# Performance work log

Measured on AMD Instinct MI355X. Metric: run time of the kernel, lower is better.

## Reference

```python
import jax, jax.numpy as jnp
import numpy as np

B, N_PROP = 2, 512
C_FEAT, FH, FW = 256, 200, 200
NUM_CLASSES, NUM_STAGES = 81, 3
POOL, SR, SCALE = 7, 2, 0.25
IMG_H, IMG_W = 800.0, 800.0
FC_DIM = 1024
IN_DIM = C_FEAT * POOL * POOL
STDS = ((0.1, 0.1, 0.2, 0.2), (0.05, 0.05, 0.1, 0.1), (0.033, 0.033, 0.067, 0.067))
CLIP_VAL = float(np.log(1000.0 / 16))
SCORE_T, NMS_T, DETS, PRE_NMS = 0.05, 0.5, 100, 2048


def bilinear(f, y, x):
    # f: [C,H,W]; y,x: [M] sample coords (torchvision roi_align bilinear rules)
    H, W = f.shape[1], f.shape[2]
    valid = (y > -1.0) & (y < H) & (x > -1.0) & (x < W)
    y = jnp.clip(y, 0.0, H - 1.0)
    x = jnp.clip(x, 0.0, W - 1.0)
    y0 = jnp.floor(y).astype(jnp.int32)
    x0 = jnp.floor(x).astype(jnp.int32)
    y1 = jnp.minimum(y0 + 1, H - 1)
    x1 = jnp.minimum(x0 + 1, W - 1)
    ly, lx = y - y0, x - x0
    hy, hx = 1.0 - ly, 1.0 - lx
    v = (hy * hx) * f[:, y0, x0] + (hy * lx) * f[:, y0, x1] \
      + (ly * hx) * f[:, y1, x0] + (ly * lx) * f[:, y1, x1]
    return v * valid  # [C,M]


def roi_align(f, rois):
    # f: [C,H,W], rois: [N,4] image coords -> [N,C,POOL,POOL]
    b = rois * SCALE
    x1, y1, x2, y2 = b[:, 0], b[:, 1], b[:, 2], b[:, 3]
    rw = jnp.maximum(x2 - x1, 1.0)
    rh = jnp.maximum(y2 - y1, 1.0)
    bw, bh = rw / POOL, rh / POOL
    p = jnp.arange(POOL, dtype=f.dtype)
    s = (jnp.arange(SR, dtype=f.dtype) + 0.5) / SR
    gy = y1[:, None, None] + (p[None, :, None] + s[None, None, :]) * bh[:, None, None]  # [N,P,SR]
    gx = x1[:, None, None] + (p[None, :, None] + s[None, None, :]) * bw[:, None, None]
    n = rois.shape[0]
    yy = jnp.broadcast_to(gy[:, :, :, None, None], (n, POOL, SR, POOL, SR))
    xx = jnp.broadcast_to(gx[:, None, None, :, :], (n, POOL, SR, POOL, SR))
    vals = bilinear(f, yy.reshape(-1), xx.reshape(-1))  # [C, N*P*SR*P*SR]
    vals = vals.reshape(f.shape[0], n, POOL, SR, POOL, SR).mean(axis=(3, 5))
    return vals.transpose(1, 0, 2, 3)


def decode_clip(props, deltas, stds):
    px1, py1, px2, py2 = props[:, 0], props[:, 1], props[:, 2], props[:, 3]
    pw = jnp.maximum(px2 - px1, 1e-6)
    ph = jnp.maximum(py2 - py1, 1e-6)
    px = px1 + 0.5 * pw
    py = py1 + 0.5 * ph
    wx, wy, ww, wh = stds
    dx = deltas[:, 0] * wx
    dy = deltas[:, 1] * wy
    dw = jnp.minimum(deltas[:, 2] * ww, CLIP_VAL)
    dh = jnp.minimum(deltas[:, 3] * wh, CLIP_VAL)
    gx = dx * pw + px
    gy = dy * ph + py
    gw = jnp.exp(dw) * pw
    gh = jnp.exp(dh) * ph
    return jnp.stack([jnp.clip(gx - 0.5 * gw, 0.0, IMG_W),
                      jnp.clip(gy - 0.5 * gh, 0.0, IMG_H),
                      jnp.clip(gx + 0.5 * gw, 0.0, IMG_W),
                      jnp.clip(gy + 0.5 * gh, 0.0, IMG_H)], axis=1)


def box_iou(a, b):
    area_a = (a[:, 2] - a[:, 0]) * (a[:, 3] - a[:, 1])
    area_b = (b[:, 2] - b[:, 0]) * (b[:, 3] - b[:, 1])
    lt = jnp.maximum(a[:, None, :2], b[None, :, :2])
    rb = jnp.minimum(a[:, None, 2:], b[None, :, 2:])
    wh = jnp.maximum(rb - lt, 0.0)
    inter = wh[..., 0] * wh[..., 1]
    return inter / (area_a[:, None] + area_b[None, :] - inter + 1e-12)


def postprocess(boxes, probs):
    # boxes [N,4], probs [N,NUM_CLASSES] -> fixed-size padded detections
    n = boxes.shape[0]
    ws = boxes[:, 2] - boxes[:, 0]
    hs = boxes[:, 3] - boxes[:, 1]
    ok = (ws >= 1.0) & (hs >= 1.0)  # remove_small_boxes(min_size=1.0)
    fg = probs[:, 1:]               # drop background (class 0)
    sc = jnp.where((fg > SCORE_T) & ok[:, None], fg, -1.0).reshape(-1)  # [N*(C-1)]
    labels = jnp.broadcast_to(jnp.arange(1, NUM_CLASSES, dtype=jnp.int32)[None, :],
                              (n, NUM_CLASSES - 1)).reshape(-1)
    bflat = jnp.broadcast_to(boxes[:, None, :], (n, NUM_CLASSES - 1, 4)).reshape(-1, 4)
    vals, idx = jax.lax.top_k(sc, PRE_NMS)  # fixed-size candidate cap, sorted desc
    bsel = bflat[idx]
    lsel = labels[idx]
    # batched_nms trick: offset boxes per label so classes never overlap
    off = bsel + (lsel.astype(bsel.dtype) * (jnp.max(bsel) + 1.0))[:, None]
    iou = box_iou(off, off)
    valid = vals > 0.0
    ar = jnp.arange(PRE_NMS)
    def body(i, keep):
        sup = (iou[i] > NMS_T) & keep[i]
        return keep & ~(sup & (ar > i))
    keep = jax.lax.fori_loop(0, PRE_NMS, body, valid)
    order = jnp.argsort(jnp.where(keep, ar, PRE_NMS + ar))[:DETS]  # kept first, score order
    kv = keep[order]
    out_boxes = jnp.where(kv[:, None], bsel[order], 0.0)
    out_scores = jnp.where(kv, vals[order], 0.0)
    out_labels = jnp.where(kv, lsel[order], 0)
    return out_boxes, out_scores, out_labels


def cascade_forward(features, proposals, W1, b1, W2, b2, Wc, bc, Wr, br):
    cur = proposals  # [B,N,4]
    logits = None
    for s in range(NUM_STAGES):
        pooled = jax.vmap(roi_align)(features, cur)  # [B,N,C,P,P]
        x = pooled.reshape(B * N_PROP, IN_DIM)
        h = jax.nn.relu(x @ W1[s] + b1[s])
        h = jax.nn.relu(h @ W2[s] + b2[s])
        logits = h @ Wc[s] + bc[s]
        deltas = (h @ Wr[s] + br[s]).reshape(B, N_PROP, 4)
        stds = STDS[s]
        cur = jax.vmap(lambda p, d: decode_clip(p, d, stds))(cur, deltas)
    probs = jax.nn.softmax(logits, axis=-1).reshape(B, N_PROP, NUM_CLASSES)
    return jax.vmap(postprocess)(cur, probs)


def setup_inputs() -> dict:
    key = jax.random.key(0)
    ks = jax.random.split(key, 12)
    features = jax.random.normal(ks[0], (B, C_FEAT, FH, FW), jnp.float32)
    cx = jax.random.uniform(ks[1], (B, N_PROP), minval=0.0, maxval=IMG_W)
    cy = jax.random.uniform(ks[2], (B, N_PROP), minval=0.0, maxval=IMG_H)
    w = jax.random.uniform(ks[3], (B, N_PROP), minval=16.0, maxval=256.0)
    h = jax.random.uniform(ks[4], (B, N_PROP), minval=16.0, maxval=256.0)
    proposals = jnp.stack([jnp.clip(cx - w / 2, 0.0, IMG_W), jnp.clip(cy - h / 2, 0.0, IMG_H),
                           jnp.clip(cx + w / 2, 0.0, IMG_W), jnp.clip(cy + h / 2, 0.0, IMG_H)],
                          axis=-1)
    def lin(k, fan_in, shape):
        return jax.random.normal(k, shape, jnp.float32) / np.sqrt(fan_in).astype(np.float32)
    W1 = lin(ks[5], IN_DIM, (NUM_STAGES, IN_DIM, FC_DIM))
    W2 = lin(ks[6], FC_DIM, (NUM_STAGES, FC_DIM, FC_DIM))
    Wc = lin(ks[7], FC_DIM, (NUM_STAGES, FC_DIM, NUM_CLASSES))
    Wr = lin(ks[8], FC_DIM, (NUM_STAGES, FC_DIM, 4)) * 0.5
    b1 = jnp.zeros((NUM_STAGES, FC_DIM), jnp.float32)
    b2 = jnp.zeros((NUM_STAGES, FC_DIM), jnp.float32)
    bc = jnp.zeros((NUM_STAGES, NUM_CLASSES), jnp.float32)
    br = jnp.zeros((NUM_STAGES, 4), jnp.float32)
    return {"features": features, "proposals": proposals, "W1": W1, "b1": b1,
            "W2": W2, "b2": b2, "Wc": Wc, "bc": bc, "Wr": Wr, "br": br}


def reference(features, proposals, W1, b1, W2, b2, Wc, bc, Wr, br):
    return cascade_forward(features, proposals, W1, b1, W2, b2, Wc, bc, Wr, br)
```

## Files before the change

kernel.cpp:

```cpp
#include <hip/hip_runtime.h>
#include <float.h>
#include <math.h>

#define NB 2
#define NPROP 512
#define NROI 1024
#define CFEAT 256
#define FH 200
#define FW 200
#define HWSZ 40000
#define INDIM 12544
#define FCD 1024
#define NCLS 81
#define NCAND 40960
#define CAP 4096
#define NSEL 2048
#define DETS 100
#define CLIPV 4.135166556742356f

#define KKT1 392
#define KKT2 32

typedef __attribute__((ext_vector_type(8))) short short8v;
typedef __attribute__((ext_vector_type(8))) unsigned short ushort8v;
typedef __attribute__((ext_vector_type(4))) float float4v;

__device__ __forceinline__ unsigned short f2bf(float x) {
    unsigned u = __float_as_uint(x);
    unsigned r = (u + 0x7fffu + ((u >> 16) & 1u)) >> 16;
    return (unsigned short)r;
}
__device__ __forceinline__ float bf2f(unsigned short b) {
    return __uint_as_float(((unsigned)b) << 16);
}
__device__ __forceinline__ void split3(float x, unsigned short& h, unsigned short& m, unsigned short& l) {
    h = f2bf(x);
    float r1 = x - bf2f(h);
    m = f2bf(r1);
    float r2 = r1 - bf2f(m);
    l = f2bf(r2);
}

__device__ __forceinline__ void gload_lds16(const void* g, void* l) {
    __builtin_amdgcn_global_load_lds((const __attribute__((address_space(1))) unsigned int*)g,
                                     (__attribute__((address_space(3))) unsigned int*)l, 16, 0, 0);
}

__device__ __forceinline__ int swz8k(int o) {
    return o ^ ((((o >> 6) ^ (o >> 8)) & 3) << 4);
}

__global__ void zero_ints_k(int* p, int n) {
    int i = blockIdx.x * blockDim.x + threadIdx.x;
    if (i < n) p[i] = 0;
}

__global__ __launch_bounds__(256) void transpose_k(const float* __restrict__ in, float* __restrict__ out) {
    __shared__ float tile[32][33];
    int b = blockIdx.z;
    int hw0 = blockIdx.x * 32;
    int c0 = blockIdx.y * 32;
    int tx = threadIdx.x;
    int ty = threadIdx.y;
#pragma unroll
    for (int i = 0; i < 32; i += 8)
        tile[ty + i][tx] = in[((size_t)(b * CFEAT + c0 + ty + i)) * HWSZ + hw0 + tx];
    __syncthreads();
#pragma unroll
    for (int i = 0; i < 32; i += 8)
        out[((size_t)b * HWSZ + hw0 + ty + i) * CFEAT + c0 + tx] = tile[tx][ty + i];
}

template<bool TRANS>
__device__ __forceinline__ float bil_sample(const float* __restrict__ feat, int b, int c,
                                            float yy, float xx) {
    bool valid = (yy > -1.f) && (yy < (float)FH) && (xx > -1.f) && (xx < (float)FW);
    float yc = fminf(fmaxf(yy, 0.f), (float)(FH - 1));
    float xc = fminf(fmaxf(xx, 0.f), (float)(FW - 1));
    int y0 = (int)floorf(yc), x0 = (int)floorf(xc);
    int y1i = min(y0 + 1, FH - 1), x1i = min(x0 + 1, FW - 1);
    float ly = yc - (float)y0, lx = xc - (float)x0;
    float hy = 1.f - ly, hx = 1.f - lx;
    float v00, v01, v10, v11;
    if (TRANS) {
        const float* base = feat + (size_t)b * HWSZ * CFEAT;
        v00 = base[((size_t)(y0 * FW + x0)) * CFEAT + c];
        v01 = base[((size_t)(y0 * FW + x1i)) * CFEAT + c];
        v10 = base[((size_t)(y1i * FW + x0)) * CFEAT + c];
        v11 = base[((size_t)(y1i * FW + x1i)) * CFEAT + c];
    } else {
        const float* base = feat + ((size_t)(b * CFEAT + c)) * HWSZ;
        v00 = base[y0 * FW + x0];
        v01 = base[y0 * FW + x1i];
        v10 = base[y1i * FW + x0];
        v11 = base[y1i * FW + x1i];
    }
    float v = hy * hx * v00 + hy * lx * v01 + ly * hx * v10 + ly * lx * v11;
    return valid ? v : 0.f;
}

template<bool TRANS>
__global__ __launch_bounds__(256) void roi_k(const float* __restrict__ feat,
                                             const float* __restrict__ boxes,
                                             float* __restrict__ xout) {
    int pp = blockIdx.x, r = blockIdx.y, c = threadIdx.x;
    int b = r >> 9;
    const float* bx = boxes + (size_t)r * 4;
    float x1 = bx[0] * 0.25f, y1 = bx[1] * 0.25f, x2 = bx[2] * 0.25f, y2 = bx[3] * 0.25f;
    float rw = fmaxf(x2 - x1, 1.0f), rh = fmaxf(y2 - y1, 1.0f);
    float bw = rw / 7.0f, bh = rh / 7.0f;
    int py = pp / 7, px = pp % 7;
    float acc = 0.f;
#pragma unroll
    for (int sy = 0; sy < 2; ++sy)
#pragma unroll
        for (int sx = 0; sx < 2; ++sx)
            acc += bil_sample<TRANS>(feat, b, c,
                                     y1 + ((float)py + 0.25f + 0.5f * (float)sy) * bh,
                                     x1 + ((float)px + 0.25f + 0.5f * (float)sx) * bw);
    xout[(size_t)r * INDIM + pp * 256 + c] = acc * 0.25f;
}

__global__ __launch_bounds__(256) void roi_split4_k(const float* __restrict__ feat,
                                                    const float* __restrict__ boxes,
                                                    unsigned short* __restrict__ Ap) {
    int tid = threadIdx.x;
    int g = tid >> 7;
    int binhalf = (tid >> 6) & 1;
    int cl = tid & 63;
    int r = blockIdx.x * 2 + g;
    int b = r >> 9;
    const float* bx = boxes + (size_t)r * 4;
    float x1 = bx[0] * 0.25f, y1 = bx[1] * 0.25f, x2 = bx[2] * 0.25f, y2 = bx[3] * 0.25f;
    float rw = fmaxf(x2 - x1, 1.0f), rh = fmaxf(y2 - y1, 1.0f);
    float bw = rw / 7.0f, bh = rh / 7.0f;
    int mt = r >> 7, rr = r & 127;
    size_t pstr = (size_t)8 * KKT1 * 4096;
    const float* base = feat + (size_t)b * HWSZ * CFEAT;
    for (int pp = binhalf; pp < 49; pp += 2) {
        int py = pp / 7, px = pp % 7;
        float ax = 0.f, ay = 0.f, az = 0.f, aw = 0.f;
#pragma unroll
        for (int sy = 0; sy < 2; ++sy) {
#pragma unroll
            for (int sx = 0; sx < 2; ++sx) {
                float yy = y1 + ((float)py + 0.25f + 0.5f * (float)sy) * bh;
                float xx = x1 + ((float)px + 0.25f + 0.5f * (float)sx) * bw;
                bool valid = (yy > -1.f) && (yy < (float)FH) && (xx > -1.f) && (xx < (float)FW);
                float yc = fminf(fmaxf(yy, 0.f), (float)(FH - 1));
                float xc = fminf(fmaxf(xx, 0.f), (float)(FW - 1));
                int y0 = (int)floorf(yc), x0 = (int)floorf(xc);
                int y1i = min(y0 + 1, FH - 1), x1i = min(x0 + 1, FW - 1);
                float ly = yc - (float)y0, lx = xc - (float)x0;
                float hy = 1.f - ly, hx = 1.f - lx;
                float w00 = hy * hx, w01 = hy * lx, w10 = ly * hx, w11 = ly * lx;
                if (!valid) { w00 = w01 = w10 = w11 = 0.f; }
                float4 v00 = ((const float4*)(base + (size_t)(y0 * FW + x0) * CFEAT))[cl];
                float4 v01 = ((const float4*)(base + (size_t)(y0 * FW + x1i) * CFEAT))[cl];
                float4 v10 = ((const float4*)(base + (size_t)(y1i * FW + x0) * CFEAT))[cl];
                float4 v11 = ((const float4*)(base + (size_t)(y1i * FW + x1i) * CFEAT))[cl];
                ax += w00 * v00.x + w01 * v01.x + w10 * v10.x + w11 * v11.x;
                ay += w00 * v00.y + w01 * v01.y + w10 * v10.y + w11 * v11.y;
                az += w00 * v00.z + w01 * v01.z + w10 * v10.z + w11 * v11.z;
                aw += w00 * v00.w + w01 * v01.w + w10 * v10.w + w11 * v11.w;
            }
        }
        ax *= 0.25f; ay *= 0.25f; az *= 0.25f; aw *= 0.25f;
        ushort4 h4, m4, l4;
        split3(ax, h4.x, m4.x, l4.x);
        split3(ay, h4.y, m4.y, l4.y);
        split3(az, h4.z, m4.z, l4.z);
        split3(aw, h4.w, m4.w, l4.w);
        int k0 = pp * 256 + cl * 4;
        int kk = k0 >> 5;
        size_t tile = ((size_t)mt * KKT1 + kk) * 4096 + rr * 32 + (k0 & 31);
        *(ushort4*)&Ap[tile] = h4;
        *(ushort4*)&Ap[tile + pstr] = m4;
        *(ushort4*)&Ap[tile + 2 * pstr] = l4;
    }
}

template<bool PERM>
__global__ __launch_bounds__(256) void wsplit_k(const float* __restrict__ W,
                                                unsigned short* __restrict__ out, int kkT) {
    __shared__ float tf[32][132];
    int nt = blockIdx.x, kk = blockIdx.y;
    int t = threadIdx.x;
    int kloc = t >> 3;
    int f4 = t & 7;
    int krow;
    if (PERM) krow = ((kk & 7) * 32 + kloc) * 49 + (kk >> 3);
    else krow = kk * 32 + kloc;
    const float* src = W + (size_t)krow * 1024 + nt * 128;
#pragma unroll
    for (int q = 0; q < 4; ++q) {
        float4 v = *(const float4*)(src + (f4 + q * 8) * 4);
        *(float4*)&tf[kloc][(f4 + q * 8) * 4] = v;
    }
    __syncthreads();
    int r = t >> 1;
    size_t tileBase = ((size_t)nt * kkT + kk) * 4096;
    size_t pstr = (size_t)8 * kkT * 4096;
#pragma unroll
    for (int cc = 0; cc < 2; ++cc) {
        int c = (t & 1) * 2 + cc;
        ushort8v hv, mv, lv;
#pragma unroll
        for (int e = 0; e < 8; ++e) {
            unsigned short h, m, l;
            split3(tf[c * 8 + e][r], h, m, l);
            hv[e] = h; mv[e] = m; lv[e] = l;
        }
        size_t o = tileBase + r * 32 + c * 8;
        *(ushort8v*)&out[o] = hv;
        *(ushort8v*)&out[o + pstr] = mv;
        *(ushort8v*)&out[o + 2 * pstr] = lv;
    }
}

__global__ __launch_bounds__(256) void wsplit_head_k(const float* __restrict__ Wc,
                                                     const float* __restrict__ Wr,
                                                     unsigned short* __restrict__ out) {
    int kk = blockIdx.x, t = threadIdx.x;
    int r = t >> 1;
    int k0 = (t & 1) * 16;
    size_t pstr = (size_t)KKT2 * 4096;
    for (int e = 0; e < 16; ++e) {
        int k = k0 + e;
        int krow = kk * 32 + k;
        float v = 0.f;
        if (r < 81) v = Wc[(size_t)krow * 81 + r];
        else if (r < 85) v = Wr[(size_t)krow * 4 + (r - 81)];
        unsigned short h, m, l;
        split3(v, h, m, l);
        size_t o = (size_t)kk * 4096 + r * 32 + k;
        out[o] = h;
        out[o + pstr] = m;
        out[o + 2 * pstr] = l;
    }
}

#define TERM16(AF) { _Pragma("unroll") for (int i = 0; i < 4; ++i) _Pragma("unroll") \
    for (int j = 0; j < 4; ++j) acc[i][j] = __builtin_amdgcn_mfma_f32_16x16x32_bf16(AF[i], bf[j], acc[i][j], 0, 0, 0); }

__global__ __launch_bounds__(256) void gemm_mfma_k(const unsigned short* __restrict__ Ap,
                                                   const unsigned short* __restrict__ Bp,
                                                   float* __restrict__ partial,
                                                   int kkT, int kkPer, int NT, int N) {
    __shared__ unsigned short sA[3][4096];
    __shared__ unsigned short sB[3][4096];
    int tid = threadIdx.x;
    int phys = blockIdx.x;
    int logical = (phys & 7) * (gridDim.x >> 3) + (phys >> 3);
    int tpc = 8 * NT;
    int xy = logical % tpc;
    int ck = logical / tpc;
    int mt = xy & 7, nt = xy >> 3;
    int kk0 = ck * kkPer;
    size_t pstrA = (size_t)8 * kkT * 4096 * 2;
    size_t pstrB = (size_t)NT * kkT * 4096 * 2;
    const char* aBase = (const char*)(Ap + (size_t)mt * kkT * 4096);
    const char* bBase = (const char*)(Bp + (size_t)nt * kkT * 4096);

    float4v acc[4][4];
#pragma unroll
    for (int i = 0; i < 4; ++i)
#pragma unroll
        for (int j = 0; j < 4; ++j) acc[i][j] = (float4v){0.f, 0.f, 0.f, 0.f};

    int lane = tid & 63, wv = tid >> 6;
    int wr = wv >> 1, wc = wv & 1;
    int ln = lane & 15;
    int q = lane >> 4;
    int qs = (q ^ (ln ^ (ln >> 2))) & 3;
    int aoffE = (wr * 64 + ln) * 32 + qs * 8;
    int boffE = (wc * 64 + ln) * 32 + qs * 8;

    int o0 = tid * 16;
    int o1 = o0 + 4096;
    int s0 = swz8k(o0);
    int s1 = swz8k(o1);

    for (int kk = kk0; kk < kk0 + kkPer; ++kk) {
        const char* at = aBase + (size_t)kk * 8192;
        const char* bt = bBase + (size_t)kk * 8192;
#pragma unroll
        for (int p = 0; p < 3; ++p) {
            gload_lds16(at + (size_t)p * pstrA + s0, (char*)sA[p] + o0);
            gload_lds16(at + (size_t)p * pstrA + s1, (char*)sA[p] + o1);
            gload_lds16(bt + (size_t)p * pstrB + s0, (char*)sB[p] + o0);
            gload_lds16(bt + (size_t)p * pstrB + s1, (char*)sB[p] + o1);
        }
        __syncthreads();
        short8v af[3][4];
#pragma unroll
        for (int p = 0; p < 3; ++p)
#pragma unroll
            for (int f = 0; f < 4; ++f)
                af[p][f] = *(const short8v*)&sA[p][aoffE + f * 512];
        short8v bf[4];
#pragma unroll
        for (int f = 0; f < 4; ++f) bf[f] = *(const short8v*)&sB[0][boffE + f * 512];
        TERM16(af[0]); TERM16(af[1]); TERM16(af[2]);
#pragma unroll
        for (int f = 0; f < 4; ++f) bf[f] = *(const short8v*)&sB[1][boffE + f * 512];
        TERM16(af[0]); TERM16(af[1]);
#pragma unroll
        for (int f = 0; f < 4; ++f) bf[f] = *(const short8v*)&sB[2][boffE + f * 512];
        TERM16(af[0]);
        __syncthreads();
    }
    float* outp = partial + (size_t)ck * 1024 * N;
    int row0 = mt * 128 + wr * 64 + (lane >> 4) * 4;
    int col = nt * 128 + wc * 64 + ln;
#pragma unroll
    for (int i = 0; i < 4; ++i)
#pragma unroll
        for (int j = 0; j < 4; ++j)
#pragma unroll
            for (int qq = 0; qq < 4; ++qq)
                outp[(size_t)(row0 + i * 16 + qq) * N + col + j * 16] = acc[i][j][qq];
}

template<int NS>
__global__ void reduce8_k(const float* __restrict__ partial, const float* __restrict__ bias,
                          unsigned short* __restrict__ planes) {
    int i = blockIdx.x * 256 + threadIdx.x;
    float s = 0.f;
#pragma unroll
    for (int c = 0; c < NS; ++c) s += partial[((size_t)c << 20) + i];
    s += bias[i & 1023];
    s = fmaxf(s, 0.f);
    int m = i >> 10, n = i & 1023;
    int mt = m >> 7, rr = m & 127, kk = n >> 5;
    unsigned short h, mm_, l;
    split3(s, h, mm_, l);
    size_t tile = ((size_t)mt * KKT2 + kk) * 4096 + rr * 32 + (n & 31);
    size_t pstr = (size_t)8 * KKT2 * 4096;
    planes[tile] = h;
    planes[tile + pstr] = mm_;
    planes[tile + 2 * pstr] = l;
}

__global__ void head_fin_k(const float* __restrict__ partial, const float* __restrict__ bc,
                           const float* __restrict__ br, float* __restrict__ logits,
                           float* __restrict__ deltas, int write_logits) {
    int idx = blockIdx.x * 256 + threadIdx.x;
    if (idx >= 1024 * 85) return;
    int m = idx / 85, col = idx - m * 85;
    float s = 0.f;
#pragma unroll
    for (int c = 0; c < 8; ++c) s += partial[(size_t)c * 131072 + m * 128 + col];
    if (col < 81) {
        if (write_logits) logits[(size_t)m * NCLS + col] = s + bc[col];
    } else {
        deltas[(size_t)m * 4 + (col - 81)] = s + br[col - 81];
    }
}

template<bool PERM>
__global__ __launch_bounds__(256) void gemm_k(const float* __restrict__ A,
                                              const float* __restrict__ Bm,
                                              float* __restrict__ partial,
                                              int K_total, int Kchunk) {
    const int M = 1024, N = 1024;
    __shared__ float As[2][16][128];
    __shared__ float Bs[2][16][64];
    int tid = threadIdx.x;
    int mb = blockIdx.x & 7;
    int nb = blockIdx.x >> 3;
    int ck = blockIdx.y;
    int k0 = ck * Kchunk;
    int am = tid >> 1;
    int ak = (tid & 1) * 8;
    int bk = tid >> 4;
    int bn = (tid & 15) * 4;
    int ty = tid >> 4, tx = tid & 15;
    const float* Aptr = A + (size_t)(mb * 128 + am) * K_total + k0 + ak;

    float acc[8][4];
#pragma unroll
    for (int i = 0; i < 8; ++i)
#pragma unroll
        for (int j = 0; j < 4; ++j) acc[i][j] = 0.f;

    auto bRowPtr = [&](int kk) -> const float* {
        int row = PERM ? ((kk & 255) * 49 + (kk >> 8)) : kk;
        return Bm + (size_t)row * N + nb * 64 + bn;
    };

    int T = Kchunk / 16;
    float4 a0 = *(const float4*)(Aptr);
    float4 a1 = *(const float4*)(Aptr + 4);
    float4 b0 = *(const float4*)bRowPtr(k0 + bk);
    As[0][ak + 0][am] = a0.x; As[0][ak + 1][am] = a0.y; As[0][ak + 2][am] = a0.z; As[0][ak + 3][am] = a0.w;
    As[0][ak + 4][am] = a1.x; As[0][ak + 5][am] = a1.y; As[0][ak + 6][am] = a1.z; As[0][ak + 7][am] = a1.w;
    *(float4*)&Bs[0][bk][bn] = b0;
    __syncthreads();

    int p = 0;
    for (int t = 0; t < T; ++t) {
        if (t + 1 < T) {
            a0 = *(const float4*)(Aptr + (t + 1) * 16);
            a1 = *(const float4*)(Aptr + (t + 1) * 16 + 4);
            b0 = *(const float4*)bRowPtr(k0 + (t + 1) * 16 + bk);
        }
#pragma unroll
        for (int k = 0; k < 16; ++k) {
            float4 av0 = *(const float4*)&As[p][k][ty * 8];
            float4 av1 = *(const float4*)&As[p][k][ty * 8 + 4];
            float4 bv = *(const float4*)&Bs[p][k][tx * 4];
            float ar[8] = {av0.x, av0.y, av0.z, av0.w, av1.x, av1.y, av1.z, av1.w};
            float br_[4] = {bv.x, bv.y, bv.z, bv.w};
#pragma unroll
            for (int i = 0; i < 8; ++i)
#pragma unroll
                for (int j = 0; j < 4; ++j) acc[i][j] = fmaf(ar[i], br_[j], acc[i][j]);
        }
        if (t + 1 < T) {
            __syncthreads();
            int qb = 1 - p;
            As[qb][ak + 0][am] = a0.x; As[qb][ak + 1][am] = a0.y; As[qb][ak + 2][am] = a0.z; As[qb][ak + 3][am] = a0.w;
            As[qb][ak + 4][am] = a1.x; As[qb][ak + 5][am] = a1.y; As[qb][ak + 6][am] = a1.z; As[qb][ak + 7][am] = a1.w;
            *(float4*)&Bs[qb][bk][bn] = b0;
            __syncthreads();
            p = qb;
        }
    }
    float* out = partial + ((size_t)ck * M + mb * 128 + ty * 8) * N + nb * 64 + tx * 4;
#pragma unroll
    for (int i = 0; i < 8; ++i) {
        float4 v = make_float4(acc[i][0], acc[i][1], acc[i][2], acc[i][3]);
        *(float4*)(out + (size_t)i * N) = v;
    }
}

__global__ void reduce4_k(const float* __restrict__ partial, const float* __restrict__ bias,
                          float* __restrict__ out) {
    const int MN = 1024 * 1024;
    int i = blockIdx.x * 256 + threadIdx.x;
    if (i >= MN) return;
    float s = partial[i] + partial[(size_t)MN + i] + partial[(size_t)2 * MN + i] + partial[(size_t)3 * MN + i];
    s += bias[i & 1023];
    out[i] = fmaxf(s, 0.f);
}

__global__ __launch_bounds__(128) void head_k(const float* __restrict__ h,
                                              const float* __restrict__ Wc, const float* __restrict__ bc,
                                              const float* __restrict__ Wr, const float* __restrict__ br,
                                              float* __restrict__ logits, float* __restrict__ deltas,
                                              int write_logits) {
    __shared__ float hs[1024];
    int m = blockIdx.x;
    int tid = threadIdx.x;
    const float4* hp = (const float4*)(h + (size_t)m * 1024);
    ((float4*)hs)[tid] = hp[tid];
    ((float4*)hs)[tid + 128] = hp[tid + 128];
    __syncthreads();
    int j = tid;
    if (j < 85) {
        bool is_cls = j < 81;
        const float* Wp = is_cls ? Wc : Wr;
        int stride = is_cls ? 81 : 4;
        int col = is_cls ? j : j - 81;
        float s0 = 0.f, s1 = 0.f, s2 = 0.f, s3 = 0.f;
        for (int k = 0; k < 1024; k += 4) {
            s0 = fmaf(hs[k + 0], Wp[(k + 0) * stride + col], s0);
            s1 = fmaf(hs[k + 1], Wp[(k + 1) * stride + col], s1);
            s2 = fmaf(hs[k + 2], Wp[(k + 2) * stride + col], s2);
            s3 = fmaf(hs[k + 3], Wp[(k + 3) * stride + col], s3);
        }
        float s = (s0 + s1) + (s2 + s3);
        if (is_cls) {
            if (write_logits) logits[(size_t)m * NCLS + col] = s + bc[col];
        } else {
            deltas[(size_t)m * 4 + col] = s + br[col];
        }
    }
}

__global__ void decode_k(const float* __restrict__ prev, const float* __restrict__ deltas,
                         float* __restrict__ nxt, float wx, float wy, float ww, float wh) {
    int r = blockIdx.x * 256 + threadIdx.x;
    if (r >= NROI) return;
    const float* p = prev + (size_t)r * 4;
    const float* d = deltas + (size_t)r * 4;
    float px1 = p[0], py1 = p[1], px2 = p[2], py2 = p[3];
    float pw = fmaxf(px2 - px1, 1e-6f), ph = fmaxf(py2 - py1, 1e-6f);
    float pcx = px1 + 0.5f * pw, pcy = py1 + 0.5f * ph;
    float dx = d[0] * wx, dy = d[1] * wy;
    float dw = fminf(d[2] * ww, CLIPV);
    float dh = fminf(d[3] * wh, CLIPV);
    float gx = dx * pw + pcx, gy = dy * ph + pcy;
    float gw = expf(dw) * pw, gh = expf(dh) * ph;
    nxt[(size_t)r * 4 + 0] = fminf(fmaxf(gx - 0.5f * gw, 0.f), 800.f);
    nxt[(size_t)r * 4 + 1] = fminf(fmaxf(gy - 0.5f * gh, 0.f), 800.f);
    nxt[(size_t)r * 4 + 2] = fminf(fmaxf(gx + 0.5f * gw, 0.f), 800.f);
    nxt[(size_t)r * 4 + 3] = fminf(fmaxf(gy + 0.5f * gh, 0.f), 800.f);
}

__global__ __launch_bounds__(128) void softmax_k(const float* __restrict__ logits, float* __restrict__ probs) {
    __shared__ float red[128];
    int m = blockIdx.x;
    int tid = threadIdx.x;
    float v = (tid < NCLS) ? logits[(size_t)m * NCLS + tid] : -FLT_MAX;
    red[tid] = v;
    __syncthreads();
    for (int o = 64; o; o >>= 1) {
        if (tid < o) red[tid] = fmaxf(red[tid], red[tid + o]);
        __syncthreads();
    }
    float mx = red[0];
    __syncthreads();
    float e = (tid < NCLS) ? expf(v - mx) : 0.f;
    red[tid] = e;
    __syncthreads();
    for (int o = 64; o; o >>= 1) {
        if (tid < o) red[tid] += red[tid + o];
        __syncthreads();
    }
    float s = red[0];
    if (tid < NCLS) probs[(size_t)m * NCLS + tid] = e / s;
}

__global__ void build_scores_k(const float* __restrict__ probs, const float* __restrict__ boxes,
                               float* __restrict__ sc, int* __restrict__ vcount) {
    int f = blockIdx.x * 256 + threadIdx.x;
    if (f >= NB * NCAND) return;
    int b = f / NCAND, ff = f % NCAND;
    int rr = ff / 80, cls = ff % 80 + 1;
    int row = b * NPROP + rr;
    const float* bx = boxes + (size_t)row * 4;
    bool ok = (bx[2] - bx[0] >= 1.f) && (bx[3] - bx[1] >= 1.f);
    float p = probs[(size_t)row * NCLS + cls];
    float s = (p > 0.05f && ok) ? p : -1.0f;
    sc[f] = s;
    if (s > 0.f) atomicAdd(&vcount[b], 1);
}

__global__ __launch_bounds__(1024) void find_pivot_k(const float* __restrict__ sc,
                                                     const int* __restrict__ vcount,
                                                     float* __restrict__ pivot) {
    int b = blockIdx.x;
    const float* s = sc + (size_t)b * NCAND;
    __shared__ int tot;
    int V = vcount[b];
    if (V <= CAP) {
        if (threadIdx.x == 0) pivot[b] = 0.f;
        return;
    }
    unsigned u = 0;
    for (int bit = 30; bit >= 0; --bit) {
        unsigned cand = u | (1u << bit);
        float cf = __uint_as_float(cand);
        if (threadIdx.x == 0) tot = 0;
        __syncthreads();
        int cnt = 0;
        for (int i = threadIdx.x; i < NCAND; i += 1024) cnt += (s[i] >= cf) ? 1 : 0;
        for (int o = 32; o; o >>= 1) cnt += __shfl_down(cnt, o);
        if ((threadIdx.x & 63) == 0) atomicAdd(&tot, cnt);
        __syncthreads();
        if (tot >= NSEL) u = cand;
        __syncthreads();
    }
    if (threadIdx.x == 0) pivot[b] = __uint_as_float(u);
}

__global__ void compact_k(const float* __restrict__ sc, const float* __restrict__ pivot,
                          float* __restrict__ ckey, int* __restrict__ cidx, int* __restrict__ ccount) {
    int f = blockIdx.x * 256 + threadIdx.x;
    if (f >= NB * NCAND) return;
    int b = f / NCAND, ff = f % NCAND;
    float s = sc[f];
    float pv = pivot[b];
    if (s > 0.f && s >= pv) {
        int slot = atomicAdd(&ccount[b], 1);
        if (slot < CAP) {
            ckey[(size_t)b * CAP + slot] = s;
            cidx[(size_t)b * CAP + slot] = ff;
        }
    }
}

__global__ __launch_bounds__(1024) void sort_select_k(const float* __restrict__ ckey,
                                                      const int* __restrict__ cidx,
                                                      const int* __restrict__ ccount,
                                                      const float* __restrict__ boxes,
                                                      float* __restrict__ selb, float* __restrict__ seloff,
                                                      float* __restrict__ selsc, int* __restrict__ sellab,
                                                      unsigned long long* __restrict__ vmask) {
    int b = blockIdx.x;
    __shared__ float ks[CAP];
    __shared__ int is[CAP];
    __shared__ float rmax[1024];
    int cnt = min(ccount[b], CAP);
    for (int i = threadIdx.x; i < CAP; i += 1024) {
        if (i < cnt) {
            ks[i] = ckey[(size_t)b * CAP + i];
            is[i] = cidx[(size_t)b * CAP + i];
        } else {
            ks[i] = -FLT_MAX;
            is[i] = 0x7FFFFFFF;
        }
    }
    __syncthreads();
    for (int k = 2; k <= CAP; k <<= 1) {
        for (int j = k >> 1; j > 0; j >>= 1) {
            for (int t = threadIdx.x; t < CAP; t += 1024) {
                int l = t ^ j;
                if (l > t) {
                    bool up = ((t & k) == 0);
                    float a = ks[t], bb = ks[l];
                    int ia = is[t], ib = is[l];
                    bool a_first = (a > bb) || (a == bb && ia < ib);
                    bool doswap = up ? !a_first : a_first;
                    if (doswap) {
                        ks[t] = bb; ks[l] = a;
                        is[t] = ib; is[l] = ia;
                    }
                }
            }
            __syncthreads();
        }
    }
    float lm = -FLT_MAX;
    for (int i = threadIdx.x; i < NSEL; i += 1024) {
        if (ks[i] > 0.f) {
            const float* bb = boxes + (size_t)(b * NPROP + is[i] / 80) * 4;
            lm = fmaxf(lm, fmaxf(fmaxf(bb[0], bb[1]), fmaxf(bb[2], bb[3])));
        }
    }
    rmax[threadIdx.x] = lm;
    __syncthreads();
    for (int o = 512; o; o >>= 1) {
        if (threadIdx.x < o) rmax[threadIdx.x] = fmaxf(rmax[threadIdx.x], rmax[threadIdx.x + o]);
        __syncthreads();
    }
    float maxb = (rmax[0] > -FLT_MAX) ? rmax[0] : 0.f;
    __syncthreads();
    for (int pass = 0; pass < 2; ++pass) {
        int i = pass * 1024 + threadIdx.x;
        bool v = ks[i] > 0.f;
        int idx = is[i];
        int rr = idx / 80;
        int cls = idx % 80 + 1;
        float b0 = 0.f, b1 = 0.f, b2 = 0.f, b3 = 0.f, offv = 0.f;
        if (v) {
            const float* bb = boxes + (size_t)(b * NPROP + rr) * 4;
            b0 = bb[0]; b1 = bb[1]; b2 = bb[2]; b3 = bb[3];
            offv = (maxb + 1.f) * (float)cls;
        }
        float* sb = selb + ((size_t)b * NSEL + i) * 4;
        sb[0] = b0; sb[1] = b1; sb[2] = b2; sb[3] = b3;
        float* so = seloff + ((size_t)b * NSEL + i) * 4;
        so[0] = b0 + offv; so[1] = b1 + offv; so[2] = b2 + offv; so[3] = b3 + offv;
        selsc[(size_t)b * NSEL + i] = v ? ks[i] : 0.f;
        sellab[(size_t)b * NSEL + i] = cls;
        unsigned long long m = __ballot(v);
        if ((threadIdx.x & 63) == 0) vmask[b * 32 + pass * 16 + (threadIdx.x >> 6)] = m;
    }
}

__global__ __launch_bounds__(256) void sup_k(const float* __restrict__ seloff,
                                             const float* __restrict__ selsc,
                                             unsigned long long* __restrict__ sup) {
    int b = blockIdx.y;
    int wave = threadIdx.x >> 6;
    int lane = threadIdx.x & 63;
    int pair = blockIdx.x * 4 + wave;
    int i = pair >> 5;
    int w = pair & 31;
    int j = w * 64 + lane;
    unsigned long long m = 0;
    if (selsc[(size_t)b * NSEL + i] > 0.f) {
        const float* oi = seloff + ((size_t)b * NSEL + i) * 4;
        const float* oj = seloff + ((size_t)b * NSEL + j) * 4;
        float ax1 = oi[0], ay1 = oi[1], ax2 = oi[2], ay2 = oi[3];
        float bx1 = oj[0], by1 = oj[1], bx2 = oj[2], by2 = oj[3];
        float areaA = (ax2 - ax1) * (ay2 - ay1);
        float areaB = (bx2 - bx1) * (by2 - by1);
        float ltx = fmaxf(ax1, bx1), lty = fmaxf(ay1, by1);
        float rbx = fminf(ax2, bx2), rby = fminf(ay2, by2);
        float iw = fmaxf(rbx - ltx, 0.f), ih = fmaxf(rby - lty, 0.f);
        float inter = iw * ih;
        float iou = inter / (areaA + areaB - inter + 1e-12f);
        m = __ballot(iou > 0.5f);
    }
    if (lane == 0) sup[((size_t)b * NSEL + i) * 32 + w] = m;
}

__global__ __launch_bounds__(256) void nms_scan_k(const unsigned long long* __restrict__ vmask,
                                                  const unsigned long long* __restrict__ sup,
                                                  const float* __restrict__ selb,
                                                  const float* __restrict__ selsc,
                                                  const int* __restrict__ sellab,
                                                  float* __restrict__ out) {
    int b = blockIdx.x;
    __shared__ unsigned long long keepw[32];
    __shared__ int pref[33];
    int tid = threadIdx.x;
    if (tid < 64) {
        int lane = tid;
        unsigned long long kw = (lane < 32) ? vmask[b * 32 + lane] : 0ull;
        for (int i = 0; i < NSEL; ++i) {
            int wi = i >> 6;
            unsigned long long wv = __shfl(kw, wi);
            if ((wv >> (i & 63)) & 1ull) {
                if (lane < 32) {
                    unsigned long long row = sup[((size_t)b * NSEL + i) * 32 + lane];
                    unsigned long long mask;
                    if (lane > wi) mask = ~0ull;
                    else if (lane == wi) mask = ((i & 63) == 63) ? 0ull : (~0ull << ((i & 63) + 1));
                    else mask = 0ull;
                    kw &= ~(row & mask);
                }
            }
        }
        if (lane < 32) keepw[lane] = kw;
    }
    __syncthreads();
    if (tid == 0) {
        int s = 0;
        for (int w = 0; w < 32; ++w) { pref[w] = s; s += __popcll(keepw[w]); }
        pref[32] = s;
    }
    __syncthreads();
    for (int i = tid; i < 600; i += 256) {
        if (i < 400) out[b * 400 + i] = 0.f;
        else if (i < 500) out[800 + b * 100 + (i - 400)] = 0.f;
        else out[1000 + b * 100 + (i - 500)] = 0.f;
    }
    __syncthreads();
    for (int e = tid; e < NSEL; e += 256) {
        int w = e >> 6;
        unsigned long long kw = keepw[w];
        if ((kw >> (e & 63)) & 1ull) {
            int rank = pref[w] + __popcll(kw & ((1ull << (e & 63)) - 1ull));
            if (rank < DETS) {
                const float* sb = selb + ((size_t)b * NSEL + e) * 4;
                out[b * 400 + rank * 4 + 0] = sb[0];
                out[b * 400 + rank * 4 + 1] = sb[1];
                out[b * 400 + rank * 4 + 2] = sb[2];
                out[b * 400 + rank * 4 + 3] = sb[3];
                out[800 + b * 100 + rank] = selsc[(size_t)b * NSEL + e];
                out[1000 + b * 100 + rank] = (float)sellab[(size_t)b * NSEL + e];
            }
        }
    }
}

extern "C" void kernel_launch(void* const* d_in, const int* in_sizes, int n_in,
                              void* d_out, int out_size, void* d_ws, size_t ws_size,
                              hipStream_t stream) {
    const float* features = (const float*)d_in[0];
    const float* proposals = (const float*)d_in[1];
    const float* W1 = (const float*)d_in[2];
    const float* b1 = (const float*)d_in[3];
    const float* W2 = (const float*)d_in[4];
    const float* b2 = (const float*)d_in[5];
    const float* Wc = (const float*)d_in[6];
    const float* bc = (const float*)d_in[7];
    const float* Wr = (const float*)d_in[8];
    const float* br = (const float*)d_in[9];

    char* ws = (char*)d_ws;
    size_t off = 0;
    auto alloc = [&](size_t bytes) -> void* {
        void* p = ws + off;
        off += (bytes + 255) & ~(size_t)255;
        return p;
    };

    float* logits = (float*)alloc((size_t)NROI * NCLS * 4);
    float* probs = (float*)alloc((size_t)NROI * NCLS * 4);
    float* deltas = (float*)alloc((size_t)NROI * 4 * 4);
    float* cur1 = (float*)alloc((size_t)NROI * 4 * 4);
    float* cur2 = (float*)alloc((size_t)NROI * 4 * 4);
    float* cur3 = (float*)alloc((size_t)NROI * 4 * 4);
    float* sc = (float*)alloc((size_t)NB * NCAND * 4);
    float* ckey = (float*)alloc((size_t)NB * CAP * 4);
    int* cidx = (int*)alloc((size_t)NB * CAP * 4);
    int* counters = (int*)alloc(256);
    float* pivot = (float*)(counters + 4);
    float* selb = (float*)alloc((size_t)NB * NSEL * 4 * 4);
    float* seloff = (float*)alloc((size_t)NB * NSEL * 4 * 4);
    float* selsc = (float*)alloc((size_t)NB * NSEL * 4);
    int* sellab = (int*)alloc((size_t)NB * NSEL * 4);
    unsigned long long* vmask = (unsigned long long*)alloc((size_t)NB * 32 * 8);
    unsigned long long* sup = (unsigned long long*)alloc((size_t)NB * NSEL * 32 * 8);

    const float stds[3][4] = {{0.1f, 0.1f, 0.2f, 0.2f},
                              {0.05f, 0.05f, 0.1f, 0.1f},
                              {0.033f, 0.033f, 0.067f, 0.067f}};
    float* curbufs[3] = {cur1, cur2, cur3};
    const float* curp = proposals;

    size_t planes1 = (size_t)3 * 8 * KKT1 * 4096 * 2;
    size_t planes2 = (size_t)3 * 8 * KKT2 * 4096 * 2;
    size_t planesH = (size_t)3 * 1 * KKT2 * 4096 * 2;
    auto mfma_need = [&](int sk) {
        return planes1 * 2 + planes2 * 3 + planesH +
               (size_t)sk * (1 << 20) * 4 +
               (size_t)NB * HWSZ * CFEAT * 4 + 65536;
    };
    int SK1 = 0;
    if (off + mfma_need(14) <= ws_size) SK1 = 14;
    else if (off + mfma_need(8) <= ws_size) SK1 = 8;

    zero_ints_k<<<1, 64, 0, stream>>>(counters, 4);

    if (SK1 > 0) {
        unsigned short* Ap1 = (unsigned short*)alloc(planes1);
        unsigned short* Bp1 = (unsigned short*)alloc(planes1);
        unsigned short* h1p = (unsigned short*)alloc(planes2);
        unsigned short* W2Tp = (unsigned short*)alloc(planes2);
        unsigned short* h2p = (unsigned short*)alloc(planes2);
        unsigned short* Whp = (unsigned short*)alloc(planesH);
        float* partial = (float*)alloc((size_t)SK1 * (1 << 20) * 4);
        float* featT = (float*)alloc((size_t)NB * HWSZ * CFEAT * 4);

        transpose_k<<<dim3(1250, 8, 2), dim3(32, 8), 0, stream>>>(features, featT);

        for (int s = 0; s < 3; ++s) {
            roi_split4_k<<<dim3(NROI / 2), 256, 0, stream>>>(featT, curp, Ap1);
            wsplit_k<true><<<dim3(8, KKT1), 256, 0, stream>>>(W1 + (size_t)s * INDIM * FCD, Bp1, KKT1);
            gemm_mfma_k<<<dim3(64 * SK1), 256, 0, stream>>>(Ap1, Bp1, partial, KKT1, KKT1 / SK1, 8, 1024);
            if (SK1 == 14)
                reduce8_k<14><<<4096, 256, 0, stream>>>(partial, b1 + s * FCD, h1p);
            else
                reduce8_k<8><<<4096, 256, 0, stream>>>(partial, b1 + s * FCD, h1p);
            wsplit_k<false><<<dim3(8, KKT2), 256, 0, stream>>>(W2 + (size_t)s * FCD * FCD, W2Tp, KKT2);
            gemm_mfma_k<<<dim3(512), 256, 0, stream>>>(h1p, W2Tp, partial, KKT2, 4, 8, 1024);
            reduce8_k<8><<<4096, 256, 0, stream>>>(partial, b2 + s * FCD, h2p);
            wsplit_head_k<<<dim3(KKT2), 256, 0, stream>>>(Wc + (size_t)s * FCD * NCLS,
                                                          Wr + (size_t)s * FCD * 4, Whp);
            gemm_mfma_k<<<dim3(64), 256, 0, stream>>>(h2p, Whp, partial, KKT2, 4, 1, 128);
            head_fin_k<<<dim3(340), 256, 0, stream>>>(partial, bc + s * NCLS, br + s * 4,
                                                      logits, deltas, (s == 2) ? 1 : 0);
            decode_k<<<4, 256, 0, stream>>>(curp, deltas, curbufs[s],
                                            stds[s][0], stds[s][1], stds[s][2], stds[s][3]);
            curp = curbufs[s];
        }
    } else {
        float* x = (float*)alloc((size_t)NROI * INDIM * 4);
        float* partial = (float*)alloc((size_t)4 * 1024 * 1024 * 4);
        float* h1 = (float*)alloc((size_t)NROI * FCD * 4);
        float* h2 = (float*)alloc((size_t)NROI * FCD * 4);
        float* featT = (float*)alloc((size_t)NB * HWSZ * CFEAT * 4);
        bool use_trans = (off <= ws_size);

        if (use_trans)
            transpose_k<<<dim3(1250, 8, 2), dim3(32, 8), 0, stream>>>(features, featT);

        for (int s = 0; s < 3; ++s) {
            if (use_trans)
                roi_k<true><<<dim3(49, 1024), 256, 0, stream>>>(featT, curp, x);
            else
                roi_k<false><<<dim3(49, 1024), 256, 0, stream>>>(features, curp, x);
            gemm_k<true><<<dim3(128, 4), 256, 0, stream>>>(x, W1 + (size_t)s * INDIM * FCD, partial, INDIM, 3136);
            reduce4_k<<<4096, 256, 0, stream>>>(partial, b1 + s * FCD, h1);
            gemm_k<false><<<dim3(128, 4), 256, 0, stream>>>(h1, W2 + (size_t)s * FCD * FCD, partial, FCD, 256);
            reduce4_k<<<4096, 256, 0, stream>>>(partial, b2 + s * FCD, h2);
            head_k<<<1024, 128, 0, stream>>>(h2, Wc + (size_t)s * FCD * NCLS, bc + s * NCLS,
                                             Wr + (size_t)s * FCD * 4, br + s * 4,
                                             logits, deltas, (s == 2) ? 1 : 0);
            decode_k<<<4, 256, 0, stream>>>(curp, deltas, curbufs[s],
                                            stds[s][0], stds[s][1], stds[s][2], stds[s][3]);
            curp = curbufs[s];
        }
    }

    softmax_k<<<1024, 128, 0, stream>>>(logits, probs);
    build_scores_k<<<320, 256, 0, stream>>>(probs, curp, sc, counters);
    find_pivot_k<<<2, 1024, 0, stream>>>(sc, counters, pivot);
    compact_k<<<320, 256, 0, stream>>>(sc, pivot, ckey, cidx, counters + 2);
    sort_select_k<<<2, 1024, 0, stream>>>(ckey, cidx, counters + 2, curp, selb, seloff, selsc, sellab, vmask);
    sup_k<<<dim3(16384, 2), 256, 0, stream>>>(seloff, selsc, sup);
    nms_scan_k<<<2, 256, 0, stream>>>(vmask, sup, selb, selsc, sellab, (float*)d_out);
}
```

Measured before the change: 1.273 ms.

## Prefetch NMS suppression rows, skip lower-triangle IoU words, fix split-K at 8

The serial NMS scan now keeps a 16-deep register ring of upcoming suppression-matrix rows. Each row's global load is issued ahead of use instead of on the dependent critical path of every kept box. The suppression-matrix kernel skips 64-box words below the diagonal, which the scan masks out anyway, roughly halving the IoU work. The first FC GEMM's split-K is fixed at 8 instead of preferring 14, which launches fewer GEMM blocks but makes the partial-sum reduction cheaper and lowers the workspace need. It also unconditionally loads all rows even for suppressed boxes, raising memory traffic and register use in the scan wave.

```diff
diff --git a/kernel.cpp b/kernel.cpp
--- a/kernel.cpp
+++ b/kernel.cpp
@@ -20,6 +20,7 @@
 
 #define KKT1 392
 #define KKT2 32
+#define SPLITK 8
 
 typedef __attribute__((ext_vector_type(8))) short short8v;
 typedef __attribute__((ext_vector_type(8))) unsigned short ushort8v;
@@ -672,7 +673,7 @@
     int w = pair & 31;
     int j = w * 64 + lane;
     unsigned long long m = 0;
-    if (selsc[(size_t)b * NSEL + i] > 0.f) {
+    if (w >= (i >> 6) && selsc[(size_t)b * NSEL + i] > 0.f) {
         const float* oi = seloff + ((size_t)b * NSEL + i) * 4;
         const float* oj = seloff + ((size_t)b * NSEL + j) * 4;
         float ax1 = oi[0], ay1 = oi[1], ax2 = oi[2], ay2 = oi[3];
@@ -702,17 +703,28 @@
     if (tid < 64) {
         int lane = tid;
         unsigned long long kw = (lane < 32) ? vmask[b * 32 + lane] : 0ull;
-        for (int i = 0; i < NSEL; ++i) {
-            int wi = i >> 6;
-            unsigned long long wv = __shfl(kw, wi);
-            if ((wv >> (i & 63)) & 1ull) {
-                if (lane < 32) {
-                    unsigned long long row = sup[((size_t)b * NSEL + i) * 32 + lane];
-                    unsigned long long mask;
-                    if (lane > wi) mask = ~0ull;
-                    else if (lane == wi) mask = ((i & 63) == 63) ? 0ull : (~0ull << ((i & 63) + 1));
-                    else mask = 0ull;
-                    kw &= ~(row & mask);
+        const unsigned long long* srow = sup + (size_t)b * NSEL * 32 + (lane & 31);
+        unsigned long long pre[16];
+#pragma unroll
+        for (int d = 0; d < 16; ++d)
+            pre[d] = (lane < 32) ? srow[(size_t)d * 32] : 0ull;
+        for (int i0 = 0; i0 < NSEL; i0 += 16) {
+#pragma unroll
+            for (int d = 0; d < 16; ++d) {
+                int i = i0 + d;
+                unsigned long long row = pre[d];
+                int nf = i + 16;
+                pre[d] = (lane < 32 && nf < NSEL) ? srow[(size_t)nf * 32] : 0ull;
+                int wi = i >> 6;
+                unsigned long long wv = __shfl(kw, wi);
+                if ((wv >> (i & 63)) & 1ull) {
+                    if (lane < 32) {
+                        unsigned long long mask;
+                        if (lane > wi) mask = ~0ull;
+                        else if (lane == wi) mask = ((i & 63) == 63) ? 0ull : (~0ull << ((i & 63) + 1));
+                        else mask = 0ull;
+                        kw &= ~(row & mask);
+                    }
                 }
             }
         }
@@ -798,25 +810,20 @@
     size_t planes1 = (size_t)3 * 8 * KKT1 * 4096 * 2;
     size_t planes2 = (size_t)3 * 8 * KKT2 * 4096 * 2;
     size_t planesH = (size_t)3 * 1 * KKT2 * 4096 * 2;
-    auto mfma_need = [&](int sk) {
-        return planes1 * 2 + planes2 * 3 + planesH +
-               (size_t)sk * (1 << 20) * 4 +
-               (size_t)NB * HWSZ * CFEAT * 4 + 65536;
-    };
-    int SK1 = 0;
-    if (off + mfma_need(14) <= ws_size) SK1 = 14;
-    else if (off + mfma_need(8) <= ws_size) SK1 = 8;
+    size_t mfma_need = planes1 * 2 + planes2 * 3 + planesH +
+                       (size_t)SPLITK * (1 << 20) * 4 +
+                       (size_t)NB * HWSZ * CFEAT * 4 + 65536;
 
     zero_ints_k<<<1, 64, 0, stream>>>(counters, 4);
 
-    if (SK1 > 0) {
+    if (off + mfma_need <= ws_size) {
         unsigned short* Ap1 = (unsigned short*)alloc(planes1);
         unsigned short* Bp1 = (unsigned short*)alloc(planes1);
         unsigned short* h1p = (unsigned short*)alloc(planes2);
         unsigned short* W2Tp = (unsigned short*)alloc(planes2);
         unsigned short* h2p = (unsigned short*)alloc(planes2);
         unsigned short* Whp = (unsigned short*)alloc(planesH);
-        float* partial = (float*)alloc((size_t)SK1 * (1 << 20) * 4);
+        float* partial = (float*)alloc((size_t)SPLITK * (1 << 20) * 4);
         float* featT = (float*)alloc((size_t)NB * HWSZ * CFEAT * 4);
 
         transpose_k<<<dim3(1250, 8, 2), dim3(32, 8), 0, stream>>>(features, featT);
@@ -824,11 +831,8 @@
         for (int s = 0; s < 3; ++s) {
             roi_split4_k<<<dim3(NROI / 2), 256, 0, stream>>>(featT, curp, Ap1);
             wsplit_k<true><<<dim3(8, KKT1), 256, 0, stream>>>(W1 + (size_t)s * INDIM * FCD, Bp1, KKT1);
-            gemm_mfma_k<<<dim3(64 * SK1), 256, 0, stream>>>(Ap1, Bp1, partial, KKT1, KKT1 / SK1, 8, 1024);
-            if (SK1 == 14)
-                reduce8_k<14><<<4096, 256, 0, stream>>>(partial, b1 + s * FCD, h1p);
-            else
-                reduce8_k<8><<<4096, 256, 0, stream>>>(partial, b1 + s * FCD, h1p);
+            gemm_mfma_k<<<dim3(64 * SPLITK), 256, 0, stream>>>(Ap1, Bp1, partial, KKT1, KKT1 / SPLITK, 8, 1024);
+            reduce8_k<SPLITK><<<4096, 256, 0, stream>>>(partial, b1 + s * FCD, h1p);
             wsplit_k<false><<<dim3(8, KKT2), 256, 0, stream>>>(W2 + (size_t)s * FCD * FCD, W2Tp, KKT2);
             gemm_mfma_k<<<dim3(512), 256, 0, stream>>>(h1p, W2Tp, partial, KKT2, 4, 8, 1024);
             reduce8_k<8><<<4096, 256, 0, stream>>>(partial, b2 + s * FCD, h2p);
```

New measurement: 1.279 ms. No clear change (+0.5%).
